# Performance work log

Measured on AMD Instinct MI355X. Metric: run time of the kernel, lower is better.

## Reference

```python
import jax, jax.numpy as jnp
from jax import lax
import numpy as np

B, CIN, L = 16, 512, 1024
COUT, K = 1024, 5          # conv out channels (GLU halves to 512), kernel size
DW = 512                    # word_feat == attn_channels == img_conv channels
HW = 196                    # 14*14 image feature locations


def setup_inputs() -> dict:
    key = jax.random.key(0)
    ks = jax.random.split(key, 8)
    s = 0.02
    return {
        "x": jax.random.normal(ks[0], (B, CIN, L), jnp.float32),
        "word_embed": jax.random.normal(ks[1], (B, L, DW), jnp.float32),
        "img_conv": jax.random.normal(ks[2], (B, DW, 14, 14), jnp.float32),
        "prev_attn": jnp.zeros((B, L, HW), jnp.float32),  # passed through, unused
        "conv_v": jax.random.normal(ks[3], (COUT, CIN, K), jnp.float32) * s,
        "conv_g": jnp.ones((COUT,), jnp.float32),
        "conv_b": jnp.zeros((COUT,), jnp.float32),
        "fc1_w": jax.random.normal(ks[4], (DW, DW), jnp.float32) * s,
        "fc1_b": jnp.zeros((DW,), jnp.float32),
        "fc2_w": jax.random.normal(ks[5], (DW, DW), jnp.float32) * s,
        "fc2_b": jnp.zeros((DW,), jnp.float32),
    }


def reference(x, word_embed, img_conv, prev_attn,
              conv_v, conv_g, conv_b, fc1_w, fc1_b, fc2_w, fc2_b):
    k = conv_v.shape[-1]
    # weight norm (PyTorch default dim=0): w = g * v / ||v||_{(in,k)}
    v_norm = jnp.sqrt(jnp.sum(conv_v * conv_v, axis=(1, 2), keepdims=True))
    w = (conv_g[:, None, None] / v_norm) * conv_v
    # Conv1d, padding=k-1 on both sides -> length L + k - 1 after ConvS2S trim
    y = lax.conv_general_dilated(x, w, window_strides=(1,),
                                 padding=[(k - 1, k - 1)],
                                 dimension_numbers=("NCH", "OIH", "NCH"))
    y = y + conv_b[None, :, None]
    # dropout is identity in eval mode
    a, b = jnp.split(y, 2, axis=1)          # GLU over channel dim
    h = a * jax.nn.sigmoid(b)
    h = h[:, :, : -(k - 1)]                  # [B, DW, L]
    identity_attn = h
    # attn_fc1 on [B, L, DW] then add word embeddings
    q = jnp.einsum("bcl,ac->bla", h, fc1_w) + fc1_b + word_embed  # [B, L, DW]
    feat = img_conv.reshape(img_conv.shape[0], img_conv.shape[1], -1)  # [B, DW, HW]
    score = jnp.einsum("bla,bap->blp", q, feat)   # [B, L, HW]
    attn = jax.nn.softmax(score, axis=-1)         # softmax over image locations
    ctx = jnp.einsum("blp,bap->bla", attn, feat)  # [B, L, DW]
    o = jnp.einsum("bla,ca->blc", ctx, fc2_w) + fc2_b
    out = o.transpose(0, 2, 1) + identity_attn
    # identity.shape == out.shape (input_feat == output_feat/2) -> no downsample
    out = out + x
    return (out, word_embed, img_conv, attn)
```

## Files before the change

### kernel.cpp

```cpp
#include <hip/hip_runtime.h>
#include <math.h>

#define NB   16
#define NCIN 512
#define NL   1024
#define NCOUT 1024
#define NK   5
#define NDW  512
#define NHW  196
#define NP   208
#define NPK  224
#define NLG  1028

typedef unsigned short ushort_t;
typedef unsigned int uint_t;
typedef __attribute__((ext_vector_type(8))) short bf16x8;
typedef __attribute__((ext_vector_type(4))) float f32x4;

static __device__ __forceinline__ ushort_t f2bf(float f) {
  uint_t u = __builtin_bit_cast(uint_t, f);
  u += 0x7fff + ((u >> 16) & 1);
  return (ushort_t)(u >> 16);
}
static __device__ __forceinline__ float bf2f(ushort_t u) {
  uint_t v = ((uint_t)u) << 16;
  return __builtin_bit_cast(float, v);
}

#define BARM()      asm volatile("s_barrier" ::: "memory")
#define WAITVM8()   asm volatile("s_waitcnt vmcnt(8)" ::: "memory")
#define WAITVM0()   asm volatile("s_waitcnt vmcnt(0)" ::: "memory")
#define WAITLGKM0() asm volatile("s_waitcnt lgkmcnt(0)" ::: "memory")

static __device__ __forceinline__ void gld16(const ushort_t* g, ushort_t* l) {
  __builtin_amdgcn_global_load_lds(
      (const __attribute__((address_space(1))) unsigned int*)g,
      (__attribute__((address_space(3))) unsigned int*)l, 16, 0, 0);
}

__global__ __launch_bounds__(256) void wnorm_kernel(
    const float* __restrict__ v, const float* __restrict__ g,
    ushort_t* __restrict__ wperm) {
  const int o = blockIdx.x;
  const float* vr = v + (size_t)o * (NCIN * NK);
  float s = 0.f;
  for (int j = threadIdx.x; j < NCIN * NK; j += 256) {
    float t = vr[j];
    s += t * t;
  }
  for (int off = 32; off; off >>= 1) s += __shfl_down(s, off, 64);
  __shared__ float red[4];
  __shared__ float scale_s;
  const int wid = threadIdx.x >> 6;
  if ((threadIdx.x & 63) == 0) red[wid] = s;
  __syncthreads();
  if (threadIdx.x == 0) {
    float tot = red[0] + red[1] + red[2] + red[3];
    scale_s = g[o] / sqrtf(tot);
  }
  __syncthreads();
  const float scale = scale_s;
  const int isB = (o >= NDW) ? 1 : 0;
  const int c = o - isB * NDW;
  const int j = (c >> 5) * 64 + isB * 32 + (c & 31);
#pragma unroll
  for (int dk = 0; dk < NK; ++dk) {
    for (int ci = threadIdx.x; ci < NCIN; ci += 256) {
      wperm[((size_t)dk * NCOUT + j) * NCIN + ci] = f2bf(vr[ci * NK + dk] * scale);
    }
  }
}

__global__ __launch_bounds__(256) void xpose_kernel(
    const float* __restrict__ x, ushort_t* __restrict__ xT) {
  const int b = blockIdx.z;
  const int ci0 = blockIdx.y * 64;
  const int l0 = blockIdx.x * 64;
  const int tid = threadIdx.x;
  __shared__ float t[64][65];
  const float* xb = x + ((size_t)b * NCIN + ci0) * NL + l0;
#pragma unroll
  for (int r = 0; r < 4; ++r) {
    int row = r * 16 + (tid >> 4);
    int col = (tid & 15) * 4;
    float4 v = *(const float4*)&xb[(size_t)row * NL + col];
    t[row][col + 0] = v.x; t[row][col + 1] = v.y;
    t[row][col + 2] = v.z; t[row][col + 3] = v.w;
  }
  __syncthreads();
  ushort_t* xo = xT + ((size_t)b * NLG + l0 + 4) * NCIN + ci0;
#pragma unroll
  for (int r = 0; r < 4; ++r) {
    int lrow = r * 16 + (tid >> 4);
    int cic = (tid & 15) * 4;
    ushort4 o4;
    o4.x = f2bf(t[cic + 0][lrow]);
    o4.y = f2bf(t[cic + 1][lrow]);
    o4.z = f2bf(t[cic + 2][lrow]);
    o4.w = f2bf(t[cic + 3][lrow]);
    *(ushort4*)&xo[(size_t)lrow * NCIN + cic] = o4;
  }
  if (blockIdx.x == 0) {
    for (int i = tid; i < 4 * 64; i += 256) {
      int rr = i >> 6, cc = i & 63;
      xT[((size_t)b * NLG + rr) * NCIN + ci0 + cc] = 0;
    }
  }
}

__global__ __launch_bounds__(256) void wcvt_kernel(
    const float* __restrict__ w1, const float* __restrict__ w2,
    ushort_t* __restrict__ w1bf, ushort_t* __restrict__ w2bf) {
  const int i = (blockIdx.x * 256 + threadIdx.x) * 4;
  {
    float4 v = *(const float4*)&w1[i];
    ushort4 o; o.x = f2bf(v.x); o.y = f2bf(v.y); o.z = f2bf(v.z); o.w = f2bf(v.w);
    *(ushort4*)&w1bf[i] = o;
  }
  {
    float4 v = *(const float4*)&w2[i];
    ushort4 o; o.x = f2bf(v.x); o.y = f2bf(v.y); o.z = f2bf(v.z); o.w = f2bf(v.w);
    *(ushort4*)&w2bf[i] = o;
  }
}

__global__ __launch_bounds__(256) void ftrans_kernel(
    const float* __restrict__ feat, ushort_t* __restrict__ fThi,
    ushort_t* __restrict__ fTlo, ushort_t* __restrict__ fbf) {
  const int b = blockIdx.y;
  const int a0 = blockIdx.x * 64;
  const int tid = threadIdx.x;
  __shared__ float t[64][200];

  const float* fb_ = feat + ((size_t)b * NDW + a0) * NHW;
#pragma unroll
  for (int pp = 0; pp < 16; ++pp) {
    int row = pp * 4 + (tid >> 6);
#pragma unroll
    for (int cc = 0; cc < 4; ++cc) {
      int col = cc * 64 + (tid & 63);
      if (col < NHW) t[row][col] = fb_[(size_t)row * NHW + col];
    }
  }
  __syncthreads();

  for (int pp = 0; pp < 13; ++pp) {
    int p = pp * 16 + (tid >> 4);
    int j = (tid & 15) * 4;
    ushort4 hi4, lo4;
#pragma unroll
    for (int k = 0; k < 4; ++k) {
      float v = (p < NHW) ? t[j + k][p] : 0.f;
      ushort_t h = f2bf(v);
      float lof = v - bf2f(h);
      ushort_t l = f2bf(lof);
      ((ushort_t*)&hi4)[k] = h;
      ((ushort_t*)&lo4)[k] = l;
    }
    size_t base = ((size_t)b * NP + p) * NDW + a0 + j;
    *(ushort4*)&fThi[base] = hi4;
    *(ushort4*)&fTlo[base] = lo4;
  }

#pragma unroll
  for (int cc = 0; cc < 4; ++cc) {
    int col = cc * 64 + (tid & 63);
    if (col < NPK) {
#pragma unroll
      for (int rr = 0; rr < 16; ++rr) {
        int al = rr * 4 + (tid >> 6);
        float v = (col < NHW) ? t[al][col] : 0.f;
        fbf[((size_t)b * NDW + a0 + al) * NPK + col] = f2bf(v);
      }
    }
  }
}

__global__ __launch_bounds__(512, 2) void conv_glu_mfma(
    const ushort_t* __restrict__ xT, const ushort_t* __restrict__ wperm,
    const float* __restrict__ conv_b, ushort_t* __restrict__ hbfT) {
  const int bb = blockIdx.x >> 2;
  const int l0 = (blockIdx.x & 3) * 256;
  const int by = blockIdx.y;
  const int tid = threadIdx.x;
  const int wid = tid >> 6;
  const int lane = tid & 63;
  const int wm = wid >> 2;
  const int wn = wid & 3;
  const int quad = lane >> 4;
  const int l16 = lane & 15;
  const int sw = (l16 & 7) << 3;
  const int csrc = ((lane & 7) ^ (lane >> 3)) << 3;

  __shared__ ushort_t sA[2][256][64];
  __shared__ ushort_t sB[2][256][64];

  f32x4 acc[8][4];
#pragma unroll
  for (int mt = 0; mt < 8; ++mt)
#pragma unroll
    for (int nt = 0; nt < 4; ++nt) acc[mt][nt] = (f32x4){0.f, 0.f, 0.f, 0.f};

  const ushort_t* gAbase = xT + (size_t)(bb * NLG + l0) * NCIN;
  const int r0 = wid * 8 + (lane >> 3);
  ushort_t* lA0 = &sA[0][0][0] + (wid * 64 + lane) * 8;
  ushort_t* lB0 = &sB[0][0][0] + (wid * 64 + lane) * 8;

  auto stage = [&](int tt, int s) {
    const int dk = tt >> 3;
    const int ci0 = (tt & 7) << 6;
    const ushort_t* gA = gAbase + (size_t)dk * NCIN + ci0 + csrc;
    const ushort_t* gB = wperm + ((size_t)dk * NCOUT + by * 256) * NCIN + ci0 + csrc;
    ushort_t* lA = lA0 + s * (256 * 64);
    ushort_t* lB = lB0 + s * (256 * 64);
#pragma unroll
    for (int c = 0; c < 4; ++c) {
      gld16(gA + (size_t)(r0 + c * 64) * NCIN, lA + c * 4096);
      gld16(gB + (size_t)(r0 + c * 64) * NCIN, lB + c * 4096);
    }
  };

  stage(0, 0);
  stage(1, 1);
  WAITVM8();
  BARM();

  for (int t = 0; t < 40; ++t) {
    const int s = t & 1;
    bf16x8 af[4][2], bfr[4][2];

#pragma unroll
    for (int mt = 0; mt < 4; ++mt)
#pragma unroll
      for (int ks = 0; ks < 2; ++ks)
        af[mt][ks] = *(const bf16x8*)&sA[s][wm * 128 + mt * 16 + l16]
                                        [(ks * 32 + quad * 8) ^ sw];
#pragma unroll
    for (int nt = 0; nt < 2; ++nt)
#pragma unroll
      for (int ks = 0; ks < 2; ++ks)
        bfr[nt][ks] = *(const bf16x8*)&sB[s][wn * 64 + nt * 16 + l16]
                                         [(ks * 32 + quad * 8) ^ sw];
    BARM();
    __builtin_amdgcn_s_setprio(1);
#pragma unroll
    for (int ks = 0; ks < 2; ++ks)
#pragma unroll
      for (int nt = 0; nt < 2; ++nt)
#pragma unroll
        for (int mt = 0; mt < 4; ++mt)
          acc[mt][nt] = __builtin_amdgcn_mfma_f32_16x16x32_bf16(
              af[mt][ks], bfr[nt][ks], acc[mt][nt], 0, 0, 0);
    __builtin_amdgcn_s_setprio(0);
    BARM();

#pragma unroll
    for (int nt = 2; nt < 4; ++nt)
#pragma unroll
      for (int ks = 0; ks < 2; ++ks)
        bfr[nt][ks] = *(const bf16x8*)&sB[s][wn * 64 + nt * 16 + l16]
                                         [(ks * 32 + quad * 8) ^ sw];
    BARM();
    __builtin_amdgcn_s_setprio(1);
#pragma unroll
    for (int ks = 0; ks < 2; ++ks)
#pragma unroll
      for (int nt = 2; nt < 4; ++nt)
#pragma unroll
        for (int mt = 0; mt < 4; ++mt)
          acc[mt][nt] = __builtin_amdgcn_mfma_f32_16x16x32_bf16(
              af[mt][ks], bfr[nt][ks], acc[mt][nt], 0, 0, 0);
    __builtin_amdgcn_s_setprio(0);
    BARM();

#pragma unroll
    for (int mt = 0; mt < 4; ++mt)
#pragma unroll
      for (int ks = 0; ks < 2; ++ks)
        af[mt][ks] = *(const bf16x8*)&sA[s][wm * 128 + (4 + mt) * 16 + l16]
                                        [(ks * 32 + quad * 8) ^ sw];
    BARM();
    __builtin_amdgcn_s_setprio(1);
#pragma unroll
    for (int ks = 0; ks < 2; ++ks)
#pragma unroll
      for (int nt = 0; nt < 2; ++nt)
#pragma unroll
        for (int mt = 0; mt < 4; ++mt)
          acc[4 + mt][nt] = __builtin_amdgcn_mfma_f32_16x16x32_bf16(
              af[mt][ks], bfr[nt][ks], acc[4 + mt][nt], 0, 0, 0);
    __builtin_amdgcn_s_setprio(0);
    WAITLGKM0();
    BARM();

    if (t < 38) stage(t + 2, s);
    __builtin_amdgcn_s_setprio(1);
#pragma unroll
    for (int ks = 0; ks < 2; ++ks)
#pragma unroll
      for (int nt = 2; nt < 4; ++nt)
#pragma unroll
        for (int mt = 0; mt < 4; ++mt)
          acc[4 + mt][nt] = __builtin_amdgcn_mfma_f32_16x16x32_bf16(
              af[mt][ks], bfr[nt][ks], acc[4 + mt][nt], 0, 0, 0);
    __builtin_amdgcn_s_setprio(0);

    if (t < 39) {
      if (t < 38) { WAITVM8(); } else { WAITVM0(); }
      BARM();
    }
  }

#pragma unroll
  for (int nt = 0; nt < 2; ++nt) {
    const int c = by * 128 + wn * 32 + nt * 16 + l16;
    const float ba = conv_b[c];
    const float bg = conv_b[c + NDW];
#pragma unroll
    for (int mt = 0; mt < 8; ++mt) {
      const int lg = l0 + wm * 128 + mt * 16 + quad * 4;
      ushort_t* ho = hbfT + ((size_t)bb * NL + lg) * NDW + c;
#pragma unroll
      for (int r = 0; r < 4; ++r) {
        float aa = acc[mt][nt][r] + ba;
        float gg = acc[mt][nt + 2][r] + bg;
        float hv = aa * (1.f / (1.f + __expf(-gg)));
        ho[(size_t)r * NDW] = f2bf(hv);
      }
    }
  }
}

__global__ __launch_bounds__(256, 2) void attn_fused(
    const ushort_t* __restrict__ hbfT, const ushort_t* __restrict__ w1bf,
    const float* __restrict__ fb1, const float* __restrict__ we,
    const ushort_t* __restrict__ fThi, const ushort_t* __restrict__ fTlo,
    const ushort_t* __restrict__ fbf, float* __restrict__ out_attn,
    ushort_t* __restrict__ ctx_bf) {
  const int b  = blockIdx.y;
  const int l0 = blockIdx.x * 64;
  const int tid = threadIdx.x;
  const int wid = tid >> 6;
  const int lane = tid & 63;
  const int quad = lane >> 4;
  const int l16 = lane & 15;
  const int s_f = ((l16 & 3) + (l16 >> 2)) & 3;
  const int wmask = (l16 & 7) << 3;

  __shared__ ushort_t smem[64000];
  ushort_t* qh = smem + 59392;
  ushort_t* ql = smem + 61696;
  ushort_t* pa = smem;

  auto stage1 = [&](int kc, int s) {
    const int a0 = kc * 32;
    ushort_t* wSb = smem + s * 16384;
    ushort_t* fhb = smem + 32768 + s * 6656;
    ushort_t* flb = smem + 46080 + s * 6656;
#pragma unroll
    for (int rr = 0; rr < 8; ++rr) {
      const int r = rr * 4 + wid;
      gld16(w1bf + (size_t)(a0 + r) * NDW + ((lane * 8) ^ ((r & 7) << 3)),
            wSb + r * 512 + lane * 8);
    }
#pragma unroll
    for (int ii = 0; ii < 4; ++ii) {
      const int i = ii * 4 + wid;
      if (i < 13) {
        const int row = i * 16 + (lane >> 2);
        const int s4 = (row + (row >> 2)) & 3;
        const size_t gsrc =
            ((size_t)b * NP + row) * NDW + a0 + (((lane & 3) * 8) ^ (s4 << 3));
        gld16(fThi + gsrc, fhb + i * 512 + lane * 8);
        gld16(fTlo + gsrc, flb + i * 512 + lane * 8);
      }
    }
  };

  uint4 hreg[16];
  {
    const ushort_t* hrow =
        hbfT + ((size_t)b * NL + l0 + wid * 16 + l16) * NDW + quad * 8;
#pragma unroll
    for (int cs = 0; cs < 16; ++cs)
      hreg[cs] = *(const uint4*)(hrow + cs * 32);
  }

  stage1(0, 0);
  __syncthreads();

  f32x4 acc[13];
#pragma unroll
  for (int nt = 0; nt < 13; ++nt) acc[nt] = (f32x4){0.f, 0.f, 0.f, 0.f};

  for (int kc = 0; kc < 16; ++kc) {
    const int cur = kc & 1;
    const ushort_t* wSc = smem + cur * 16384;
    const ushort_t* fhc = smem + 32768 + cur * 6656;
    const ushort_t* flc = smem + 46080 + cur * 6656;
    const int a0 = kc * 32;

    float wev[2][4], bias[2];
#pragma unroll
    for (int nt = 0; nt < 2; ++nt) {
      const int a = a0 + nt * 16 + l16;
      bias[nt] = fb1[a];
#pragma unroll
      for (int r = 0; r < 4; ++r) {
        const int l = l0 + wid * 16 + quad * 4 + r;
        wev[nt][r] = we[((size_t)b * NL + l) * NDW + a];
      }
    }

    if (kc < 15) stage1(kc + 1, cur ^ 1);

    f32x4 aq[2][2];
    aq[0][0] = aq[0][1] = aq[1][0] = aq[1][1] = (f32x4){0.f, 0.f, 0.f, 0.f};
#pragma unroll
    for (int cs = 0; cs < 16; ++cs) {
      bf16x8 af = __builtin_bit_cast(bf16x8, hreg[cs]);
#pragma unroll
      for (int nt = 0; nt < 2; ++nt) {
        bf16x8 bw = *(const bf16x8*)&wSc[(nt * 16 + l16) * 512 +
                                         ((cs * 32 + quad * 8) ^ wmask)];
        aq[cs & 1][nt] = __builtin_amdgcn_mfma_f32_16x16x32_bf16(af, bw, aq[cs & 1][nt], 0, 0, 0);
      }
    }
#pragma unroll
    for (int nt = 0; nt < 2; ++nt) {
#pragma unroll
      for (int r = 0; r < 4; ++r) {
        float qv = aq[0][nt][r] + aq[1][nt][r] + bias[nt] + wev[nt][r];
        ushort_t h = f2bf(qv);
        const int row = wid * 16 + quad * 4 + r;
        qh[row * 36 + nt * 16 + l16] = h;
        ql[row * 36 + nt * 16 + l16] = f2bf(qv - bf2f(h));
      }
    }
    WAITLGKM0();
    __builtin_amdgcn_sched_barrier(0);

    bf16x8 ah = *(const bf16x8*)&qh[(wid * 16 + l16) * 36 + quad * 8];
    bf16x8 al = *(const bf16x8*)&ql[(wid * 16 + l16) * 36 + quad * 8];
    const int fcol = (quad * 8) ^ (s_f << 3);
#pragma unroll
    for (int nt = 0; nt < 13; ++nt) {
      bf16x8 bh = *(const bf16x8*)&fhc[(nt * 16 + l16) * 32 + fcol];
      bf16x8 bl = *(const bf16x8*)&flc[(nt * 16 + l16) * 32 + fcol];
      acc[nt] = __builtin_amdgcn_mfma_f32_16x16x32_bf16(ah, bh, acc[nt], 0, 0, 0);
      acc[nt] = __builtin_amdgcn_mfma_f32_16x16x32_bf16(al, bh, acc[nt], 0, 0, 0);
      acc[nt] = __builtin_amdgcn_mfma_f32_16x16x32_bf16(ah, bl, acc[nt], 0, 0, 0);
    }

    if (kc < 15) {
      WAITLGKM0();
      WAITVM0();
      BARM();
    }
  }

  const bool v12 = (l16 < 4);
#pragma unroll
  for (int r = 0; r < 4; ++r) {
    float mx = -1e30f;
#pragma unroll
    for (int nt = 0; nt < 12; ++nt) mx = fmaxf(mx, acc[nt][r]);
    if (v12) mx = fmaxf(mx, acc[12][r]);
#pragma unroll
    for (int off = 1; off < 16; off <<= 1) mx = fmaxf(mx, __shfl_xor(mx, off, 16));
    float ex[13];
    float sum = 0.f;
#pragma unroll
    for (int nt = 0; nt < 12; ++nt) { ex[nt] = __expf(acc[nt][r] - mx); sum += ex[nt]; }
    ex[12] = v12 ? __expf(acc[12][r] - mx) : 0.f;
    sum += ex[12];
#pragma unroll
    for (int off = 1; off < 16; off <<= 1) sum += __shfl_xor(sum, off, 16);
    const float inv = 1.f / sum;
    const int l = l0 + wid * 16 + quad * 4 + r;
    float* ao = out_attn + ((size_t)b * NL + l) * NHW;
#pragma unroll
    for (int nt = 0; nt < 13; ++nt) {
      float av = ex[nt] * inv;
      acc[nt][r] = av;
      int p = nt * 16 + l16;
      if (p < NHW) ao[p] = av;
    }
  }

  __syncthreads();

  auto stage2 = [&](int ac, int s) {
    const int a0c = ac * 32;
    ushort_t* fbb = smem + 14848 + s * 7168;
#pragma unroll
    for (int ii = 0; ii < 4; ++ii) {
      const int i = ii * 4 + wid;
      if (i < 14) {
        const int byte0 = i * 1024 + lane * 16;
        const unsigned q64 = (unsigned)byte0 >> 6;
        const int row = (int)(q64 / 7u);
        const int colb = (int)(q64 - (unsigned)row * 7u) * 64 + (byte0 & 63);
        const int cu = colb >> 1;
        const int s4 = (row + (row >> 2)) & 3;
        gld16(fbf + ((size_t)b * NDW + a0c + row) * NPK + (cu ^ (s4 << 3)),
              fbb + i * 512 + lane * 8);
      }
    }
  };

#pragma unroll
  for (int r = 0; r < 4; ++r) {
    const int row = wid * 16 + quad * 4 + r;
#pragma unroll
    for (int nt = 0; nt < 13; ++nt) {
      int p = nt * 16 + l16;
      pa[row * 232 + p] = (p < NHW) ? f2bf(acc[nt][r]) : (ushort_t)0;
    }
    pa[row * 232 + 208 + l16] = 0;
  }
  stage2(0, 0);
  __syncthreads();

  for (int ac = 0; ac < 16; ++ac) {
    const int cur = ac & 1;
    const ushort_t* fbc = smem + 14848 + cur * 7168;
    if (ac < 15) stage2(ac + 1, cur ^ 1);

    f32x4 ca[2];
    ca[0] = ca[1] = (f32x4){0.f, 0.f, 0.f, 0.f};
#pragma unroll
    for (int ks = 0; ks < 7; ++ks) {
      bf16x8 af = *(const bf16x8*)&pa[(wid * 16 + l16) * 232 + ks * 32 + quad * 8];
#pragma unroll
      for (int nt = 0; nt < 2; ++nt) {
        bf16x8 bv = *(const bf16x8*)&fbc[(nt * 16 + l16) * 224 +
                                         ((ks * 32 + quad * 8) ^ (s_f << 3))];
        ca[nt] = __builtin_amdgcn_mfma_f32_16x16x32_bf16(af, bv, ca[nt], 0, 0, 0);
      }
    }
#pragma unroll
    for (int nt = 0; nt < 2; ++nt) {
      const int a = ac * 32 + nt * 16 + l16;
#pragma unroll
      for (int r = 0; r < 4; ++r) {
        const int l = l0 + wid * 16 + quad * 4 + r;
        ctx_bf[((size_t)b * NL + l) * NDW + a] = f2bf(ca[nt][r]);
      }
    }
    if (ac < 15) {
      WAITLGKM0();
      WAITVM0();
      BARM();
    }
  }
}

__global__ __launch_bounds__(256, 2) void fc2_mfma(
    const ushort_t* __restrict__ w2bf, const ushort_t* __restrict__ ctx_bf,
    const float* __restrict__ fb2, const ushort_t* __restrict__ hbfT,
    const float* __restrict__ x, float* __restrict__ out0) {
  const int b  = blockIdx.z;
  const int c0 = blockIdx.y * 128;
  const int l0 = blockIdx.x * 128;
  const int tid = threadIdx.x;
  const int wid = tid >> 6;
  const int lane = tid & 63;
  const int wl = wid & 1;
  const int wc = wid >> 1;
  const int quad = lane >> 4;
  const int l16 = lane & 15;

  __shared__ ushort_t la[128][72];
  __shared__ ushort_t lb[128][72];

  f32x4 acc[4][4];
#pragma unroll
  for (int mt = 0; mt < 4; ++mt)
#pragma unroll
    for (int nt = 0; nt < 4; ++nt) acc[mt][nt] = (f32x4){0.f, 0.f, 0.f, 0.f};

  for (int a0 = 0; a0 < NDW; a0 += 64) {
    __syncthreads();
#pragma unroll
    for (int it = 0; it < 4; ++it) {
      int t = tid + it * 256;
      int r = t >> 3, seg = t & 7;
      *(uint4*)&la[r][seg * 8] = *(const uint4*)(w2bf + (size_t)(c0 + r) * NDW + a0 + seg * 8);
    }
#pragma unroll
    for (int it = 0; it < 4; ++it) {
      int t = tid + it * 256;
      int r = t >> 3, seg = t & 7;
      *(uint4*)&lb[r][seg * 8] =
          *(const uint4*)(ctx_bf + ((size_t)b * NL + l0 + r) * NDW + a0 + seg * 8);
    }
    __syncthreads();
#pragma unroll
    for (int ks = 0; ks < 2; ++ks) {
      bf16x8 af[4];
#pragma unroll
      for (int mt = 0; mt < 4; ++mt)
        af[mt] = *(const bf16x8*)&la[wl * 64 + mt * 16 + l16][ks * 32 + quad * 8];
#pragma unroll
      for (int nt = 0; nt < 4; ++nt) {
        bf16x8 bf = *(const bf16x8*)&lb[wc * 64 + nt * 16 + l16][ks * 32 + quad * 8];
#pragma unroll
        for (int mt = 0; mt < 4; ++mt)
          acc[mt][nt] = __builtin_amdgcn_mfma_f32_16x16x32_bf16(af[mt], bf, acc[mt][nt], 0, 0, 0);
      }
    }
  }

#pragma unroll
  for (int mt = 0; mt < 4; ++mt) {
    const int cb = c0 + wl * 64 + mt * 16 + quad * 4;
    float4 bias4 = *(const float4*)&fb2[cb];
#pragma unroll
    for (int nt = 0; nt < 4; ++nt) {
      const int l = l0 + wc * 64 + nt * 16 + l16;
      ushort4 h4 = *(const ushort4*)&hbfT[((size_t)b * NL + l) * NDW + cb];
      const float bias[4] = {bias4.x, bias4.y, bias4.z, bias4.w};
      const ushort_t hs[4] = {h4.x, h4.y, h4.z, h4.w};
#pragma unroll
      for (int r = 0; r < 4; ++r) {
        size_t idx = ((size_t)b * NDW + cb + r) * NL + l;
        out0[idx] = acc[mt][nt][r] + bias[r] + bf2f(hs[r]) + x[idx];
      }
    }
  }
}

extern "C" void kernel_launch(void* const* d_in, const int* in_sizes, int n_in,
                              void* d_out, int out_size, void* d_ws, size_t ws_size,
                              hipStream_t stream) {
  const float* x      = (const float*)d_in[0];
  const float* we     = (const float*)d_in[1];
  const float* img    = (const float*)d_in[2];
  const float* conv_v = (const float*)d_in[4];
  const float* conv_g = (const float*)d_in[5];
  const float* conv_b = (const float*)d_in[6];
  const float* fc1_w  = (const float*)d_in[7];
  const float* fc1_b  = (const float*)d_in[8];
  const float* fc2_w  = (const float*)d_in[9];
  const float* fc2_b  = (const float*)d_in[10];

  float* out0     = (float*)d_out;
  float* out_we   = out0 + 8388608;
  float* out_img  = out_we + 8388608;
  float* out_attn = out_img + 1605632;

  ushort_t* wsu = (ushort_t*)d_ws;
  ushort_t* wperm = wsu;
  ushort_t* xT    = wsu + 2621440;
  ushort_t* ctx_b = wsu;
  ushort_t* hbfT  = wsu + 16777216;
  ushort_t* w1bf  = wsu + 25165824;
  ushort_t* w2bf  = wsu + 25165824 + 262144;
  ushort_t* fThi  = wsu + 25690112;
  ushort_t* fTlo  = wsu + 27394048;
  ushort_t* fbf   = wsu + 29097984;

  wnorm_kernel<<<dim3(NCOUT), 256, 0, stream>>>(conv_v, conv_g, wperm);
  xpose_kernel<<<dim3(16, 8, NB), 256, 0, stream>>>(x, xT);
  wcvt_kernel<<<dim3(256), 256, 0, stream>>>(fc1_w, fc2_w, w1bf, w2bf);
  ftrans_kernel<<<dim3(8, NB), 256, 0, stream>>>(img, fThi, fTlo, fbf);

  conv_glu_mfma<<<dim3(64, 4), 512, 0, stream>>>(xT, wperm, conv_b, hbfT);
  attn_fused<<<dim3(16, NB), 256, 0, stream>>>(hbfT, w1bf, fc1_b, we,
                                               fThi, fTlo, fbf, out_attn, ctx_b);
  fc2_mfma<<<dim3(8, 4, NB), 256, 0, stream>>>(w2bf, ctx_b, fc2_b, hbfT, x, out0);

  hipMemcpyAsync(out_we, we, (size_t)8388608 * sizeof(float),
                 hipMemcpyDeviceToDevice, stream);
  hipMemcpyAsync(out_img, img, (size_t)1605632 * sizeof(float),
                 hipMemcpyDeviceToDevice, stream);
}
```

Before: 391.6 us.

## Double-buffer fc2 GEMM with async LDS loads, fold weight conversion, widen ftrans

```diff
diff --git a/kernel.cpp b/kernel.cpp
--- a/kernel.cpp
+++ b/kernel.cpp
@@ -40,7 +40,9 @@
 
 __global__ __launch_bounds__(256) void wnorm_kernel(
     const float* __restrict__ v, const float* __restrict__ g,
-    ushort_t* __restrict__ wperm) {
+    ushort_t* __restrict__ wperm,
+    const float* __restrict__ w1, const float* __restrict__ w2,
+    ushort_t* __restrict__ w1bf, ushort_t* __restrict__ w2bf) {
   const int o = blockIdx.x;
   const float* vr = v + (size_t)o * (NCIN * NK);
   float s = 0.f;
@@ -69,6 +71,19 @@
       wperm[((size_t)dk * NCOUT + j) * NCIN + ci] = f2bf(vr[ci * NK + dk] * scale);
     }
   }
+  if (o < 256) {
+    const int i = (o * 256 + threadIdx.x) * 4;
+    {
+      float4 vv = *(const float4*)&w1[i];
+      ushort4 oo; oo.x = f2bf(vv.x); oo.y = f2bf(vv.y); oo.z = f2bf(vv.z); oo.w = f2bf(vv.w);
+      *(ushort4*)&w1bf[i] = oo;
+    }
+    {
+      float4 vv = *(const float4*)&w2[i];
+      ushort4 oo; oo.x = f2bf(vv.x); oo.y = f2bf(vv.y); oo.z = f2bf(vv.z); oo.w = f2bf(vv.w);
+      *(ushort4*)&w2bf[i] = oo;
+    }
+  }
 }
 
 __global__ __launch_bounds__(256) void xpose_kernel(
@@ -108,23 +123,7 @@
   }
 }
 
-__global__ __launch_bounds__(256) void wcvt_kernel(
-    const float* __restrict__ w1, const float* __restrict__ w2,
-    ushort_t* __restrict__ w1bf, ushort_t* __restrict__ w2bf) {
-  const int i = (blockIdx.x * 256 + threadIdx.x) * 4;
-  {
-    float4 v = *(const float4*)&w1[i];
-    ushort4 o; o.x = f2bf(v.x); o.y = f2bf(v.y); o.z = f2bf(v.z); o.w = f2bf(v.w);
-    *(ushort4*)&w1bf[i] = o;
-  }
-  {
-    float4 v = *(const float4*)&w2[i];
-    ushort4 o; o.x = f2bf(v.x); o.y = f2bf(v.y); o.z = f2bf(v.z); o.w = f2bf(v.w);
-    *(ushort4*)&w2bf[i] = o;
-  }
-}
-
-__global__ __launch_bounds__(256) void ftrans_kernel(
+__global__ __launch_bounds__(512) void ftrans_kernel(
     const float* __restrict__ feat, ushort_t* __restrict__ fThi,
     ushort_t* __restrict__ fTlo, ushort_t* __restrict__ fbf) {
   const int b = blockIdx.y;
@@ -134,8 +133,8 @@
 
   const float* fb_ = feat + ((size_t)b * NDW + a0) * NHW;
 #pragma unroll
-  for (int pp = 0; pp < 16; ++pp) {
-    int row = pp * 4 + (tid >> 6);
+  for (int pp = 0; pp < 8; ++pp) {
+    int row = pp * 8 + (tid >> 6);
 #pragma unroll
     for (int cc = 0; cc < 4; ++cc) {
       int col = cc * 64 + (tid & 63);
@@ -145,21 +144,20 @@
   __syncthreads();
 
   for (int pp = 0; pp < 13; ++pp) {
-    int p = pp * 16 + (tid >> 4);
-    int j = (tid & 15) * 4;
-    ushort4 hi4, lo4;
-#pragma unroll
-    for (int k = 0; k < 4; ++k) {
+    int p = pp * 16 + (tid >> 5);
+    int j = (tid & 31) * 2;
+    ushort2 hi2, lo2;
+#pragma unroll
+    for (int k = 0; k < 2; ++k) {
       float v = (p < NHW) ? t[j + k][p] : 0.f;
       ushort_t h = f2bf(v);
       float lof = v - bf2f(h);
-      ushort_t l = f2bf(lof);
-      ((ushort_t*)&hi4)[k] = h;
-      ((ushort_t*)&lo4)[k] = l;
+      ((ushort_t*)&hi2)[k] = h;
+      ((ushort_t*)&lo2)[k] = f2bf(lof);
     }
     size_t base = ((size_t)b * NP + p) * NDW + a0 + j;
-    *(ushort4*)&fThi[base] = hi4;
-    *(ushort4*)&fTlo[base] = lo4;
+    *(ushort2*)&fThi[base] = hi2;
+    *(ushort2*)&fTlo[base] = lo2;
   }
 
 #pragma unroll
@@ -167,8 +165,8 @@
     int col = cc * 64 + (tid & 63);
     if (col < NPK) {
 #pragma unroll
-      for (int rr = 0; rr < 16; ++rr) {
-        int al = rr * 4 + (tid >> 6);
+      for (int rr = 0; rr < 8; ++rr) {
+        int al = rr * 8 + (tid >> 6);
         float v = (col < NHW) ? t[al][col] : 0.f;
         fbf[((size_t)b * NDW + a0 + al) * NPK + col] = f2bf(v);
       }
@@ -570,9 +568,11 @@
   const int wc = wid >> 1;
   const int quad = lane >> 4;
   const int l16 = lane & 15;
-
-  __shared__ ushort_t la[128][72];
-  __shared__ ushort_t lb[128][72];
+  const int sw = (l16 & 7) << 3;
+  const int csrc = ((lane & 7) ^ (lane >> 3)) << 3;
+
+  __shared__ ushort_t sA[2][128][64];
+  __shared__ ushort_t sB[2][128][64];
 
   f32x4 acc[4][4];
 #pragma unroll
@@ -580,35 +580,59 @@
 #pragma unroll
     for (int nt = 0; nt < 4; ++nt) acc[mt][nt] = (f32x4){0.f, 0.f, 0.f, 0.f};
 
-  for (int a0 = 0; a0 < NDW; a0 += 64) {
-    __syncthreads();
-#pragma unroll
-    for (int it = 0; it < 4; ++it) {
-      int t = tid + it * 256;
-      int r = t >> 3, seg = t & 7;
-      *(uint4*)&la[r][seg * 8] = *(const uint4*)(w2bf + (size_t)(c0 + r) * NDW + a0 + seg * 8);
-    }
-#pragma unroll
-    for (int it = 0; it < 4; ++it) {
-      int t = tid + it * 256;
-      int r = t >> 3, seg = t & 7;
-      *(uint4*)&lb[r][seg * 8] =
-          *(const uint4*)(ctx_bf + ((size_t)b * NL + l0 + r) * NDW + a0 + seg * 8);
-    }
-    __syncthreads();
-#pragma unroll
-    for (int ks = 0; ks < 2; ++ks) {
-      bf16x8 af[4];
-#pragma unroll
-      for (int mt = 0; mt < 4; ++mt)
-        af[mt] = *(const bf16x8*)&la[wl * 64 + mt * 16 + l16][ks * 32 + quad * 8];
-#pragma unroll
-      for (int nt = 0; nt < 4; ++nt) {
-        bf16x8 bf = *(const bf16x8*)&lb[wc * 64 + nt * 16 + l16][ks * 32 + quad * 8];
+  const ushort_t* gA = w2bf + (size_t)c0 * NDW;
+  const ushort_t* gB = ctx_bf + ((size_t)b * NL + l0) * NDW;
+  const int r0 = wid * 8 + (lane >> 3);
+  ushort_t* lA0 = &sA[0][0][0] + wid * 512 + lane * 8;
+  ushort_t* lB0 = &sB[0][0][0] + wid * 512 + lane * 8;
+
+  auto stage = [&](int t, int s) {
+    const int a0 = t * 64;
+    ushort_t* lA = lA0 + s * (128 * 64);
+    ushort_t* lB = lB0 + s * (128 * 64);
+#pragma unroll
+    for (int c = 0; c < 4; ++c) {
+      gld16(gA + (size_t)(r0 + c * 32) * NDW + a0 + csrc, lA + c * 2048);
+      gld16(gB + (size_t)(r0 + c * 32) * NDW + a0 + csrc, lB + c * 2048);
+    }
+  };
+
+  stage(0, 0);
+  stage(1, 1);
+  WAITVM8();
+  BARM();
+
+  for (int t = 0; t < 8; ++t) {
+    const int s = t & 1;
+    bf16x8 af[4][2], bfr[4][2];
+#pragma unroll
+    for (int mt = 0; mt < 4; ++mt)
+#pragma unroll
+      for (int ks = 0; ks < 2; ++ks)
+        af[mt][ks] = *(const bf16x8*)&sA[s][wl * 64 + mt * 16 + l16]
+                                        [(ks * 32 + quad * 8) ^ sw];
+#pragma unroll
+    for (int nt = 0; nt < 4; ++nt)
+#pragma unroll
+      for (int ks = 0; ks < 2; ++ks)
+        bfr[nt][ks] = *(const bf16x8*)&sB[s][wc * 64 + nt * 16 + l16]
+                                         [(ks * 32 + quad * 8) ^ sw];
+    WAITLGKM0();
+    BARM();
+    if (t < 6) stage(t + 2, s);
+    __builtin_amdgcn_s_setprio(1);
+#pragma unroll
+    for (int ks = 0; ks < 2; ++ks)
+#pragma unroll
+      for (int nt = 0; nt < 4; ++nt)
 #pragma unroll
         for (int mt = 0; mt < 4; ++mt)
-          acc[mt][nt] = __builtin_amdgcn_mfma_f32_16x16x32_bf16(af[mt], bf, acc[mt][nt], 0, 0, 0);
-      }
+          acc[mt][nt] = __builtin_amdgcn_mfma_f32_16x16x32_bf16(
+              af[mt][ks], bfr[nt][ks], acc[mt][nt], 0, 0, 0);
+    __builtin_amdgcn_s_setprio(0);
+    if (t < 7) {
+      if (t < 6) { WAITVM8(); } else { WAITVM0(); }
+      BARM();
     }
   }
 
@@ -661,10 +685,10 @@
   ushort_t* fTlo  = wsu + 27394048;
   ushort_t* fbf   = wsu + 29097984;
 
-  wnorm_kernel<<<dim3(NCOUT), 256, 0, stream>>>(conv_v, conv_g, wperm);
+  wnorm_kernel<<<dim3(NCOUT), 256, 0, stream>>>(conv_v, conv_g, wperm,
+                                                fc1_w, fc2_w, w1bf, w2bf);
   xpose_kernel<<<dim3(16, 8, NB), 256, 0, stream>>>(x, xT);
-  wcvt_kernel<<<dim3(256), 256, 0, stream>>>(fc1_w, fc2_w, w1bf, w2bf);
-  ftrans_kernel<<<dim3(8, NB), 256, 0, stream>>>(img, fThi, fTlo, fbf);
+  ftrans_kernel<<<dim3(8, NB), 512, 0, stream>>>(img, fThi, fTlo, fbf);
 
   conv_glu_mfma<<<dim3(64, 4), 512, 0, stream>>>(xT, wperm, conv_b, hbfT);
   attn_fused<<<dim3(16, NB), 256, 0, stream>>>(hbfT, w1bf, fc1_b, we,
```

New measurement: 356.0 us. 9.1% less time.
